# Kernel optimization log

Hardware: AMD Instinct MI355X
Metric: run time of the kernel (lower is better)

Reference implementation:

```python
import jax, jax.numpy as jnp
import numpy as np


def fwht(x):
    """Normalized fast Walsh-Hadamard transform along last dim (== matmul_hadU).
    x[..., n] with n a power of 2; returns H_n @ x / sqrt(n) (Sylvester ordering).
    """
    orig_shape = x.shape
    n = orig_shape[-1]
    x = x.reshape(-1, n)
    h = 1
    while h < n:
        # pair elements at distance h: butterfly (a+b, a-b)
        x = x.reshape(-1, n // (2 * h), 2, h)
        a = x[:, :, 0:1, :]
        b = x[:, :, 1:2, :]
        x = jnp.concatenate([a + b, a - b], axis=2).reshape(-1, n)
        h *= 2
    scale = jnp.asarray(1.0 / np.sqrt(n), x.dtype)
    return (x * scale).reshape(orig_shape)


def setup_inputs() -> dict:
    key = jax.random.key(0)
    k1, k2, k3 = jax.random.split(key, 3)
    B, S, D_IN, D_OUT = 4, 2048, 4096, 4096
    x = jax.random.normal(k1, (B, S, D_IN), dtype=jnp.float32)
    W = jax.random.normal(k2, (D_OUT, D_IN), dtype=jnp.float32) * (1.0 / np.sqrt(D_IN))
    b = jax.random.normal(k3, (D_OUT,), dtype=jnp.float32)
    return {"x": x, "W": W, "b": b}


def reference(x, W, b):
    # Hadamard rotation of the activations, then Linear: y = fwht(x) @ W.T + b
    rotated = fwht(x)                                   # [B, S, D_in]
    return jnp.einsum("bsd,od->bso", rotated, W) + b    # [B, S, D_out]
```

## Files before the change

kernel.cpp:

```cpp
#include <hip/hip_runtime.h>
#include <hip/hip_bf16.h>
#include <cstdint>
#include <cstddef>

typedef __bf16 bf16_t;
typedef bf16_t bf16x8 __attribute__((ext_vector_type(8)));
typedef float  f32x4  __attribute__((ext_vector_type(4)));

#define FWHT_N 4096

#define BM 256
#define BN 256
#define KSTEP 32
#define ABYTES 16384
#define BUFBYTES 32768
#define NBUF 4

__device__ __forceinline__ void fwht16(float v[16]) {
#pragma unroll
    for (int h = 1; h < 16; h <<= 1) {
#pragma unroll
        for (int i = 0; i < 16; ++i) {
            if (!(i & h)) {
                const float a = v[i];
                const float b = v[i | h];
                v[i]     = a + b;
                v[i | h] = a - b;
            }
        }
    }
}

__device__ __forceinline__ int pad(int i) { return i + (i >> 5); }

__global__ __launch_bounds__(256) void fwht_rows_bf16(const float* __restrict__ W,
                                                      bf16_t* __restrict__ Wt) {
    __shared__ float lds[FWHT_N + (FWHT_N >> 5)];
    const int r = blockIdx.x;
    const int t = threadIdx.x;

    float v[16];

    const float4* src = (const float4*)(W + (size_t)r * FWHT_N + 16 * t);
    {
        const float4 a0 = src[0], a1 = src[1], a2 = src[2], a3 = src[3];
        v[0] = a0.x; v[1] = a0.y; v[2]  = a0.z; v[3]  = a0.w;
        v[4] = a1.x; v[5] = a1.y; v[6]  = a1.z; v[7]  = a1.w;
        v[8] = a2.x; v[9] = a2.y; v[10] = a2.z; v[11] = a2.w;
        v[12] = a3.x; v[13] = a3.y; v[14] = a3.z; v[15] = a3.w;
    }
    fwht16(v);
    {
        const int base = 16 * t + (t >> 1);
#pragma unroll
        for (int k = 0; k < 16; ++k) lds[base + k] = v[k];
    }
    __syncthreads();

    const int b1 = ((t >> 4) << 8) | (t & 15);
#pragma unroll
    for (int k = 0; k < 16; ++k) v[k] = lds[pad(b1 + (k << 4))];
    fwht16(v);
#pragma unroll
    for (int k = 0; k < 16; ++k) lds[pad(b1 + (k << 4))] = v[k];
    __syncthreads();

#pragma unroll
    for (int k = 0; k < 16; ++k) v[k] = lds[pad(t + (k << 8))];
    fwht16(v);

    const float s = 0.015625f;
    bf16_t* dst = Wt + (size_t)r * FWHT_N + t;
#pragma unroll
    for (int k = 0; k < 16; ++k) dst[k << 8] = (bf16_t)(v[k] * s);
}

__global__ __launch_bounds__(256) void cvt_f32_bf16(const float4* __restrict__ x,
                                                    bf16x8* __restrict__ y) {
    const size_t i = (size_t)blockIdx.x * 256 + threadIdx.x;
    const float4 a = x[2 * i];
    const float4 b = x[2 * i + 1];
    bf16x8 o;
    o[0] = (bf16_t)a.x; o[1] = (bf16_t)a.y; o[2] = (bf16_t)a.z; o[3] = (bf16_t)a.w;
    o[4] = (bf16_t)b.x; o[5] = (bf16_t)b.y; o[6] = (bf16_t)b.z; o[7] = (bf16_t)b.w;
    y[i] = o;
}

__device__ __forceinline__ void g2lds16(const bf16_t* g, bf16_t* l) {
    __builtin_amdgcn_global_load_lds((__attribute__((address_space(1))) void*)g,
                                     (__attribute__((address_space(3))) void*)l,
                                     16, 0, 0);
}

__global__ __launch_bounds__(512, 2) void gemm256_bt_bias(
    const bf16_t* __restrict__ A,
    const bf16_t* __restrict__ Bm,
    const float* __restrict__ bias,
    float* __restrict__ C,
    int M, int N, int K)
{
    __shared__ __align__(16) char lds[NBUF * BUFBYTES];

    const int tid  = threadIdx.x;
    const int wave = tid >> 6;
    const int lane = tid & 63;
    const int quad = lane >> 4;
    const int l16  = lane & 15;

    const int m0 = blockIdx.y * BM;
    const int n0 = blockIdx.x * BN;
    const int wm = (wave >> 2) * 128;
    const int wn = (wave & 3) * 64;

    const int srow = wave * 16 + (lane >> 2);
    const int scb  = (((lane & 3) ^ ((lane >> 3) & 3)) << 4);
    const int L0   = wave * 1024 + lane * 16;

    const bf16_t* gA0 = A  + (size_t)(m0 + srow)       * K + (scb >> 1);
    const bf16_t* gA1 = A  + (size_t)(m0 + srow + 128) * K + (scb >> 1);
    const bf16_t* gB0 = Bm + (size_t)(n0 + srow)       * K + (scb >> 1);
    const bf16_t* gB1 = Bm + (size_t)(n0 + srow + 128) * K + (scb >> 1);

    const int cbr   = ((quad ^ ((lane >> 1) & 3)) << 4);
    const int aoff  = l16 * 64 + cbr;
    const int abase = ((wm >> 4) << 10) + aoff;
    const int bbase = ABYTES + ((wn >> 4) << 10) + aoff;

    f32x4 acc[8][4] = {};

    const int NT = K / KSTEP;

    auto stage = [&](int s) {
        char* d = &lds[(s & (NBUF - 1)) * BUFBYTES];
        const int ko = s * KSTEP;
        g2lds16(gA0 + ko, (bf16_t*)(d + L0));
        g2lds16(gA1 + ko, (bf16_t*)(d + L0 + 8192));
        g2lds16(gB0 + ko, (bf16_t*)(d + ABYTES + L0));
        g2lds16(gB1 + ko, (bf16_t*)(d + ABYTES + L0 + 8192));
    };

    stage(0);
    stage(1);
    asm volatile("s_waitcnt vmcnt(4)" ::: "memory");
    __builtin_amdgcn_s_barrier();
    __builtin_amdgcn_sched_barrier(0);

#pragma unroll 2
    for (int s = 0; s < NT; ++s) {
        if (s + 2 < NT) stage(s + 2);

        const char* buf = &lds[(s & (NBUF - 1)) * BUFBYTES];
        bf16x8 bfr[4], af[8];
#pragma unroll
        for (int ni = 0; ni < 4; ++ni)
            bfr[ni] = *(const bf16x8*)(buf + bbase + (ni << 10));
#pragma unroll
        for (int mi = 0; mi < 8; ++mi)
            af[mi] = *(const bf16x8*)(buf + abase + (mi << 10));

        __builtin_amdgcn_s_setprio(1);
#pragma unroll
        for (int mi = 0; mi < 8; ++mi)
#pragma unroll
            for (int ni = 0; ni < 4; ++ni)
                acc[mi][ni] = __builtin_amdgcn_mfma_f32_16x16x32_bf16(
                    af[mi], bfr[ni], acc[mi][ni], 0, 0, 0);
        __builtin_amdgcn_s_setprio(0);

        if (s + 1 < NT) {
            if (s + 2 < NT) { asm volatile("s_waitcnt vmcnt(4)" ::: "memory"); }
            else            { asm volatile("s_waitcnt vmcnt(0)" ::: "memory"); }
            __builtin_amdgcn_s_barrier();
            __builtin_amdgcn_sched_barrier(0);
        }
    }

    const int crow = quad * 4;
#pragma unroll
    for (int ni = 0; ni < 4; ++ni) {
        const int n  = n0 + wn + ni * 16 + l16;
        const float bv = bias[n];
#pragma unroll
        for (int mi = 0; mi < 8; ++mi) {
            const int mb = m0 + wm + mi * 16 + crow;
#pragma unroll
            for (int r = 0; r < 4; ++r)
                C[(size_t)(mb + r) * N + n] = acc[mi][ni][r] + bv;
        }
    }
}

extern "C" void kernel_launch(void* const* d_in, const int* in_sizes, int n_in,
                              void* d_out, int out_size, void* d_ws, size_t ws_size,
                              hipStream_t stream) {
    const float* x = (const float*)d_in[0];
    const float* W = (const float*)d_in[1];
    const float* b = (const float*)d_in[2];
    float* out = (float*)d_out;

    const int K = 4096;
    const int N = 4096;
    const int M = in_sizes[0] / K;

    bf16_t* xb = (bf16_t*)d_ws;
    bf16_t* Wt = xb + (size_t)M * K;

    hipLaunchKernelGGL(fwht_rows_bf16, dim3(N), dim3(256), 0, stream, W, Wt);

    const int cvt_blocks = (int)(((size_t)M * K) / 8 / 256);
    hipLaunchKernelGGL(cvt_f32_bf16, dim3(cvt_blocks), dim3(256), 0, stream,
                       (const float4*)x, (bf16x8*)xb);

    hipLaunchKernelGGL(gemm256_bt_bias, dim3(N / BN, M / BM), dim3(512), 0, stream,
                       xb, Wt, b, out, M, N, K);
}
```

Measured before the change: 509.8 us.

## Double-buffer register fragments in GEMM loop and swizzle block order

Restructures the GEMM main loop so the LDS-to-register fragment loads for the next k-step are issued before the MFMAs of the current step. Two register fragment sets are used, and global-to-LDS staging runs three steps ahead with clamped indices for the tail. It also remaps block indices so consecutive blocks are spread across eight groups, aiming for better L2 locality or XCD distribution. The aim is to hide LDS read latency behind matrix math. In exchange it raises register pressure, does redundant clamped tail loads, and shortens the LDS buffer reuse distance, which could introduce races.

Result: faster. 492.1 us (-3.5%).

```diff
diff --git a/kernel.cpp b/kernel.cpp
--- a/kernel.cpp
+++ b/kernel.cpp
@@ -107,8 +107,13 @@
     const int quad = lane >> 4;
     const int l16  = lane & 15;
 
-    const int m0 = blockIdx.y * BM;
-    const int n0 = blockIdx.x * BN;
+    const int nbx  = N / BN;
+    const int flat = blockIdx.y * nbx + blockIdx.x;
+    const int per  = (nbx * (M / BM)) >> 3;
+    const int nf   = (flat & 7) * per + (flat >> 3);
+    const int m0   = (nf / nbx) * BM;
+    const int n0   = (nf % nbx) * BN;
+
     const int wm = (wave >> 2) * 128;
     const int wn = (wave & 3) * 64;
 
@@ -127,53 +132,64 @@
     const int bbase = ABYTES + ((wn >> 4) << 10) + aoff;
 
     f32x4 acc[8][4] = {};
+    bf16x8 aF0[8], bF0[4], aF1[8], bF1[4];
 
     const int NT = K / KSTEP;
 
-    auto stage = [&](int s) {
+    auto stageTo = [&](int s) {
         char* d = &lds[(s & (NBUF - 1)) * BUFBYTES];
-        const int ko = s * KSTEP;
+        const int ko = (s < NT ? s : NT - 1) * KSTEP;
         g2lds16(gA0 + ko, (bf16_t*)(d + L0));
         g2lds16(gA1 + ko, (bf16_t*)(d + L0 + 8192));
         g2lds16(gB0 + ko, (bf16_t*)(d + ABYTES + L0));
         g2lds16(gB1 + ko, (bf16_t*)(d + ABYTES + L0 + 8192));
     };
-
-    stage(0);
-    stage(1);
+    auto loadFrags = [&](int s, bf16x8 (&fa)[8], bf16x8 (&fb)[4]) {
+        const int sc = (s < NT ? s : NT - 1);
+        const char* buf = &lds[(sc & (NBUF - 1)) * BUFBYTES];
+#pragma unroll
+        for (int ni = 0; ni < 4; ++ni)
+            fb[ni] = *(const bf16x8*)(buf + bbase + (ni << 10));
+#pragma unroll
+        for (int mi = 0; mi < 8; ++mi)
+            fa[mi] = *(const bf16x8*)(buf + abase + (mi << 10));
+    };
+    auto mfmaAll = [&](bf16x8 (&fa)[8], bf16x8 (&fb)[4]) {
+        __builtin_amdgcn_s_setprio(1);
+#pragma unroll
+        for (int mi = 0; mi < 8; ++mi)
+#pragma unroll
+            for (int ni = 0; ni < 4; ++ni)
+                acc[mi][ni] = __builtin_amdgcn_mfma_f32_16x16x32_bf16(
+                    fa[mi], fb[ni], acc[mi][ni], 0, 0, 0);
+        __builtin_amdgcn_s_setprio(0);
+    };
+
+    stageTo(0);
+    stageTo(1);
     asm volatile("s_waitcnt vmcnt(4)" ::: "memory");
     __builtin_amdgcn_s_barrier();
     __builtin_amdgcn_sched_barrier(0);
-
-#pragma unroll 2
-    for (int s = 0; s < NT; ++s) {
-        if (s + 2 < NT) stage(s + 2);
-
-        const char* buf = &lds[(s & (NBUF - 1)) * BUFBYTES];
-        bf16x8 bfr[4], af[8];
-#pragma unroll
-        for (int ni = 0; ni < 4; ++ni)
-            bfr[ni] = *(const bf16x8*)(buf + bbase + (ni << 10));
-#pragma unroll
-        for (int mi = 0; mi < 8; ++mi)
-            af[mi] = *(const bf16x8*)(buf + abase + (mi << 10));
-
-        __builtin_amdgcn_s_setprio(1);
-#pragma unroll
-        for (int mi = 0; mi < 8; ++mi)
-#pragma unroll
-            for (int ni = 0; ni < 4; ++ni)
-                acc[mi][ni] = __builtin_amdgcn_mfma_f32_16x16x32_bf16(
-                    af[mi], bfr[ni], acc[mi][ni], 0, 0, 0);
-        __builtin_amdgcn_s_setprio(0);
-
-        if (s + 1 < NT) {
-            if (s + 2 < NT) { asm volatile("s_waitcnt vmcnt(4)" ::: "memory"); }
-            else            { asm volatile("s_waitcnt vmcnt(0)" ::: "memory"); }
-            __builtin_amdgcn_s_barrier();
-            __builtin_amdgcn_sched_barrier(0);
-        }
-    }
+    loadFrags(0, aF0, bF0);
+    stageTo(2);
+
+#pragma unroll 1
+    for (int s = 0; s < NT; s += 2) {
+        asm volatile("s_waitcnt vmcnt(4)" ::: "memory");
+        __builtin_amdgcn_s_barrier();
+        __builtin_amdgcn_sched_barrier(0);
+        loadFrags(s + 1, aF1, bF1);
+        stageTo(s + 3);
+        mfmaAll(aF0, bF0);
+
+        asm volatile("s_waitcnt vmcnt(4)" ::: "memory");
+        __builtin_amdgcn_s_barrier();
+        __builtin_amdgcn_sched_barrier(0);
+        loadFrags(s + 2, aF0, bF0);
+        stageTo(s + 4);
+        mfmaAll(aF1, bF1);
+    }
+    asm volatile("s_waitcnt vmcnt(0)" ::: "memory");
 
     const int crow = quad * 4;
 #pragma unroll
```
